# Performance work log

Hardware: AMD Instinct MI355X
Metric: run time of the kernel (lower is better)

Reference implementation:

```python
import jax, jax.numpy as jnp
import numpy as np

N, F_IN, H, W = 8192, 512, 256, 64
THRESHOLD = 0.8


def setup_inputs() -> dict:
    key = jax.random.key(0)
    ks = jax.random.split(key, 9)
    def lin(k, fan_in, shape):
        return (jax.random.normal(k, shape, jnp.float32) / np.sqrt(fan_in)).astype(jnp.float32)
    return {
        "state_batch": jax.random.normal(ks[0], (N, F_IN), jnp.float32),
        "W1": lin(ks[1], F_IN, (F_IN, H)), "b1": jnp.zeros((H,), jnp.float32),
        "W2": lin(ks[2], H, (H, H)),      "b2": jnp.zeros((H,), jnp.float32),
        "Wq": lin(ks[3], H, (H, W)),      "bq": jnp.zeros((W,), jnp.float32),
        "Wh": lin(ks[4], W, (W, 1)),      "bh": jnp.zeros((1,), jnp.float32),
    }


def reference(state_batch, W1, b1, W2, b2, Wq, bq, Wh, bh):
    # classical encoder: two ReLU Linear layers
    enc = jax.nn.relu(state_batch @ W1 + b1)
    enc = jax.nn.relu(enc @ W2 + b2)
    # quantum layer surrogate: bounded features in [-1, 1] like PauliZ expectations
    q_out = jnp.tanh(enc @ Wq + bq)                      # [N, W]

    # pairwise squared-cosine fidelity (vectorized Gram matrix, replaces
    # the itertools.combinations + .item() host-sync loop)
    qn = q_out / (jnp.linalg.norm(q_out, axis=1, keepdims=True) + 1e-12)
    fid = (qn @ qn.T) ** 2                               # [N, N]

    n = q_out.shape[0]
    # graph edges: fid >= threshold, no self loops; edge weight = 1.0
    mask = (fid >= THRESHOLD) & (~jnp.eye(n, dtype=bool))
    deg = mask.sum(axis=1)
    wsum = mask.astype(q_out.dtype).sum(axis=1)          # all weights are 1.0
    # mean neighbor weight; nodes with no neighbors keep their own feature (factor 1)
    mean_w = jnp.where(deg > 0, wsum / jnp.maximum(deg, 1).astype(q_out.dtype), 1.0)
    attn = q_out * mean_w[:, None]                       # [N, W]

    agg = attn.sum(axis=0, keepdims=True)                # [1, W]
    out = (agg @ Wh + bh).squeeze(-1)                    # [1]
    return out
```

## Files before the change

kernel.cpp:

```cpp
#include <hip/hip_runtime.h>
#include <hip/hip_bf16.h>
#include <math.h>


#define N_ROWS 8192
#define F_IN   512
#define H_DIM  256
#define W_DIM  64

#define LDW 72
#define LDE 280

#define W1_E (F_IN * H_DIM)
#define W2_E (H_DIM * H_DIM)
#define WQ_E (H_DIM * W_DIM)
#define W_BLOCKS ((W1_E + W2_E + WQ_E + 255) / 256)

using bf16x8 = __attribute__((ext_vector_type(8))) short;
using bf16x4 = __attribute__((ext_vector_type(4))) short;
using f32x4  = __attribute__((ext_vector_type(4))) float;
typedef __hip_bfloat16 bf16;

__device__ __forceinline__ void split2(float v, bf16& hi, bf16& lo) {
    bf16 h = __float2bfloat16(v);
    hi = h;
    lo = __float2bfloat16(v - __bfloat162float(h));
}

__global__ __launch_bounds__(256) void prep_w(
    const float* __restrict__ W1, const float* __restrict__ W2,
    const float* __restrict__ Wq, const float* __restrict__ bh,
    bf16* __restrict__ W1h, bf16* __restrict__ W1l,
    bf16* __restrict__ W2h, bf16* __restrict__ W2l,
    bf16* __restrict__ Wqh, bf16* __restrict__ Wql,
    float* __restrict__ out)
{
    if (blockIdx.x == 0 && threadIdx.x == 0) out[0] = bh[0];
    int gid = blockIdx.x * 256 + threadIdx.x;
    if (gid < W1_E) {
        int k = gid >> 8, n = gid & 255;
        split2(W1[gid], W1h[n * F_IN + k], W1l[n * F_IN + k]);
        return;
    }
    gid -= W1_E;
    if (gid < W2_E) {
        int k = gid >> 8, n = gid & 255;
        split2(W2[gid], W2h[n * H_DIM + k], W2l[n * H_DIM + k]);
        return;
    }
    gid -= W2_E;
    if (gid < WQ_E) {
        int k = gid >> 6, n = gid & 63;
        split2(Wq[gid], Wqh[n * H_DIM + k], Wql[n * H_DIM + k]);
    }
}

__global__ __launch_bounds__(512) void fused_chain(
    const float* __restrict__ S,
    const bf16* __restrict__ W1h, const bf16* __restrict__ W1l,
    const bf16* __restrict__ W2h, const bf16* __restrict__ W2l,
    const bf16* __restrict__ Wqh, const bf16* __restrict__ Wql,
    const float* __restrict__ b1, const float* __restrict__ b2,
    const float* __restrict__ bq, const float* __restrict__ Wh,
    float* __restrict__ out)
{
    __shared__ bf16 Ssh[32 * LDW];
    __shared__ bf16 Ssl[32 * LDW];
    __shared__ bf16 Bsh[256 * LDW];
    __shared__ bf16 Bsl[256 * LDW];
    __shared__ bf16 E1h[32 * LDE];
    __shared__ bf16 E1l[32 * LDE];
    __shared__ bf16 E2h[32 * LDE];
    __shared__ bf16 E2l[32 * LDE];
    __shared__ float red[2][64];

    const int t = threadIdx.x;
    const int w = t >> 6, quad = (t & 63) >> 4, m16 = t & 15;
    const int row0 = blockIdx.x * 32;

    f32x4 acc[2][2] = {};
    {
        const int srow = t >> 4, scol = (t & 15) << 2;
        float4 sv;
        bf16x8 wv[8];
        sv = *(const float4*)(S + (size_t)(row0 + srow) * F_IN + scol);
        #pragma unroll
        for (int i = 0; i < 8; ++i) {
            const int c = t + 512 * i, pl = c >> 11, cp = c & 2047;
            const int n = cp >> 3, sg = (cp & 7) << 3;
            wv[i] = *(const bf16x8*)((pl ? W1l : W1h) + (size_t)n * F_IN + sg);
        }
        for (int k0 = 0; k0 < F_IN; k0 += 64) {
            __syncthreads();
            {
                bf16 hb[4], lb[4];
                split2(sv.x, hb[0], lb[0]); split2(sv.y, hb[1], lb[1]);
                split2(sv.z, hb[2], lb[2]); split2(sv.w, hb[3], lb[3]);
                *(bf16x4*)&Ssh[srow * LDW + scol] = *(const bf16x4*)hb;
                *(bf16x4*)&Ssl[srow * LDW + scol] = *(const bf16x4*)lb;
            }
            #pragma unroll
            for (int i = 0; i < 8; ++i) {
                const int c = t + 512 * i, pl = c >> 11, cp = c & 2047;
                const int n = cp >> 3, sg = (cp & 7) << 3;
                *(bf16x8*)&(pl ? Bsl : Bsh)[n * LDW + sg] = wv[i];
            }
            __syncthreads();
            if (k0 + 64 < F_IN) {
                sv = *(const float4*)(S + (size_t)(row0 + srow) * F_IN + k0 + 64 + scol);
                #pragma unroll
                for (int i = 0; i < 8; ++i) {
                    const int c = t + 512 * i, pl = c >> 11, cp = c & 2047;
                    const int n = cp >> 3, sg = (cp & 7) << 3;
                    wv[i] = *(const bf16x8*)((pl ? W1l : W1h) + (size_t)n * F_IN + k0 + 64 + sg);
                }
            }
            #pragma unroll
            for (int kk = 0; kk < 64; kk += 32) {
                bf16x8 a0h = *(const bf16x8*)(&Ssh[m16 * LDW + kk + quad * 8]);
                bf16x8 a0l = *(const bf16x8*)(&Ssl[m16 * LDW + kk + quad * 8]);
                bf16x8 a1h = *(const bf16x8*)(&Ssh[(16 + m16) * LDW + kk + quad * 8]);
                bf16x8 a1l = *(const bf16x8*)(&Ssl[(16 + m16) * LDW + kk + quad * 8]);
                #pragma unroll
                for (int jj = 0; jj < 2; ++jj) {
                    const int bn = (32 * w + jj * 16 + m16) * LDW + kk + quad * 8;
                    bf16x8 b_h = *(const bf16x8*)(&Bsh[bn]);
                    bf16x8 b_l = *(const bf16x8*)(&Bsl[bn]);
                    acc[0][jj] = __builtin_amdgcn_mfma_f32_16x16x32_bf16(a0h, b_h, acc[0][jj], 0, 0, 0);
                    acc[0][jj] = __builtin_amdgcn_mfma_f32_16x16x32_bf16(a0l, b_h, acc[0][jj], 0, 0, 0);
                    acc[0][jj] = __builtin_amdgcn_mfma_f32_16x16x32_bf16(a0h, b_l, acc[0][jj], 0, 0, 0);
                    acc[1][jj] = __builtin_amdgcn_mfma_f32_16x16x32_bf16(a1h, b_h, acc[1][jj], 0, 0, 0);
                    acc[1][jj] = __builtin_amdgcn_mfma_f32_16x16x32_bf16(a1l, b_h, acc[1][jj], 0, 0, 0);
                    acc[1][jj] = __builtin_amdgcn_mfma_f32_16x16x32_bf16(a1h, b_l, acc[1][jj], 0, 0, 0);
                }
            }
        }
        #pragma unroll
        for (int i = 0; i < 2; ++i)
            #pragma unroll
            for (int jj = 0; jj < 2; ++jj) {
                const int c = 32 * w + jj * 16 + m16;
                const float bv = b1[c];
                #pragma unroll
                for (int r = 0; r < 4; ++r) {
                    const int rr = i * 16 + quad * 4 + r;
                    float vv = fmaxf(acc[i][jj][r] + bv, 0.0f);
                    split2(vv, E1h[rr * LDE + c], E1l[rr * LDE + c]);
                }
            }
    }

    {
        bf16x8 wv[8];
        #pragma unroll
        for (int i = 0; i < 8; ++i) {
            const int c = t + 512 * i, pl = c >> 11, cp = c & 2047;
            const int n = cp >> 3, sg = (cp & 7) << 3;
            wv[i] = *(const bf16x8*)((pl ? W2l : W2h) + (size_t)n * H_DIM + sg);
        }
        #pragma unroll
        for (int i = 0; i < 2; ++i)
            #pragma unroll
            for (int jj = 0; jj < 2; ++jj)
                acc[i][jj] = (f32x4){0.f, 0.f, 0.f, 0.f};
        for (int k0 = 0; k0 < H_DIM; k0 += 64) {
            __syncthreads();
            #pragma unroll
            for (int i = 0; i < 8; ++i) {
                const int c = t + 512 * i, pl = c >> 11, cp = c & 2047;
                const int n = cp >> 3, sg = (cp & 7) << 3;
                *(bf16x8*)&(pl ? Bsl : Bsh)[n * LDW + sg] = wv[i];
            }
            __syncthreads();
            if (k0 + 64 < H_DIM) {
                #pragma unroll
                for (int i = 0; i < 8; ++i) {
                    const int c = t + 512 * i, pl = c >> 11, cp = c & 2047;
                    const int n = cp >> 3, sg = (cp & 7) << 3;
                    wv[i] = *(const bf16x8*)((pl ? W2l : W2h) + (size_t)n * H_DIM + k0 + 64 + sg);
                }
            }
            #pragma unroll
            for (int kk = 0; kk < 64; kk += 32) {
                bf16x8 a0h = *(const bf16x8*)(&E1h[m16 * LDE + k0 + kk + quad * 8]);
                bf16x8 a0l = *(const bf16x8*)(&E1l[m16 * LDE + k0 + kk + quad * 8]);
                bf16x8 a1h = *(const bf16x8*)(&E1h[(16 + m16) * LDE + k0 + kk + quad * 8]);
                bf16x8 a1l = *(const bf16x8*)(&E1l[(16 + m16) * LDE + k0 + kk + quad * 8]);
                #pragma unroll
                for (int jj = 0; jj < 2; ++jj) {
                    const int bn = (32 * w + jj * 16 + m16) * LDW + kk + quad * 8;
                    bf16x8 b_h = *(const bf16x8*)(&Bsh[bn]);
                    bf16x8 b_l = *(const bf16x8*)(&Bsl[bn]);
                    acc[0][jj] = __builtin_amdgcn_mfma_f32_16x16x32_bf16(a0h, b_h, acc[0][jj], 0, 0, 0);
                    acc[0][jj] = __builtin_amdgcn_mfma_f32_16x16x32_bf16(a0l, b_h, acc[0][jj], 0, 0, 0);
                    acc[0][jj] = __builtin_amdgcn_mfma_f32_16x16x32_bf16(a0h, b_l, acc[0][jj], 0, 0, 0);
                    acc[1][jj] = __builtin_amdgcn_mfma_f32_16x16x32_bf16(a1h, b_h, acc[1][jj], 0, 0, 0);
                    acc[1][jj] = __builtin_amdgcn_mfma_f32_16x16x32_bf16(a1l, b_h, acc[1][jj], 0, 0, 0);
                    acc[1][jj] = __builtin_amdgcn_mfma_f32_16x16x32_bf16(a1h, b_l, acc[1][jj], 0, 0, 0);
                }
            }
        }
        #pragma unroll
        for (int i = 0; i < 2; ++i)
            #pragma unroll
            for (int jj = 0; jj < 2; ++jj) {
                const int c = 32 * w + jj * 16 + m16;
                const float bv = b2[c];
                #pragma unroll
                for (int r = 0; r < 4; ++r) {
                    const int rr = i * 16 + quad * 4 + r;
                    float vv = fmaxf(acc[i][jj][r] + bv, 0.0f);
                    split2(vv, E2h[rr * LDE + c], E2l[rr * LDE + c]);
                }
            }
    }

    {
        const int rf = w >> 2, cf = w & 3;
        f32x4 acc3 = {0.f, 0.f, 0.f, 0.f};
        bf16x8 wq[2];
        #pragma unroll
        for (int i = 0; i < 2; ++i) {
            const int c = t + 512 * i, pl = c >> 9, cp = c & 511;
            const int n = cp >> 3, sg = (cp & 7) << 3;
            wq[i] = *(const bf16x8*)((pl ? Wql : Wqh) + (size_t)n * H_DIM + sg);
        }
        for (int k0 = 0; k0 < H_DIM; k0 += 64) {
            __syncthreads();
            #pragma unroll
            for (int i = 0; i < 2; ++i) {
                const int c = t + 512 * i, pl = c >> 9, cp = c & 511;
                const int n = cp >> 3, sg = (cp & 7) << 3;
                *(bf16x8*)&(pl ? Bsl : Bsh)[n * LDW + sg] = wq[i];
            }
            __syncthreads();
            if (k0 + 64 < H_DIM) {
                #pragma unroll
                for (int i = 0; i < 2; ++i) {
                    const int c = t + 512 * i, pl = c >> 9, cp = c & 511;
                    const int n = cp >> 3, sg = (cp & 7) << 3;
                    wq[i] = *(const bf16x8*)((pl ? Wql : Wqh) + (size_t)n * H_DIM + k0 + 64 + sg);
                }
            }
            #pragma unroll
            for (int kk = 0; kk < 64; kk += 32) {
                bf16x8 a_h = *(const bf16x8*)(&E2h[(rf * 16 + m16) * LDE + k0 + kk + quad * 8]);
                bf16x8 a_l = *(const bf16x8*)(&E2l[(rf * 16 + m16) * LDE + k0 + kk + quad * 8]);
                const int bn = (cf * 16 + m16) * LDW + kk + quad * 8;
                bf16x8 b_h = *(const bf16x8*)(&Bsh[bn]);
                bf16x8 b_l = *(const bf16x8*)(&Bsl[bn]);
                acc3 = __builtin_amdgcn_mfma_f32_16x16x32_bf16(a_h, b_h, acc3, 0, 0, 0);
                acc3 = __builtin_amdgcn_mfma_f32_16x16x32_bf16(a_l, b_h, acc3, 0, 0, 0);
                acc3 = __builtin_amdgcn_mfma_f32_16x16x32_bf16(a_h, b_l, acc3, 0, 0, 0);
            }
        }
        const int c = cf * 16 + m16;
        const float bv = bq[c];
        float v = 0.f;
        #pragma unroll
        for (int r = 0; r < 4; ++r)
            v += tanhf(acc3[r] + bv);
        v += __shfl_xor(v, 16, 64);
        v += __shfl_xor(v, 32, 64);
        if (quad == 0) red[rf][c] = v;
        __syncthreads();
        if (t < W_DIM) {
            float s = (red[0][t] + red[1][t]) * Wh[t];
            #pragma unroll
            for (int o = 32; o > 0; o >>= 1) s += __shfl_down(s, o);
            if (t == 0) atomicAdd(out, s);
        }
    }
}

extern "C" void kernel_launch(void* const* d_in, const int* in_sizes, int n_in,
                              void* d_out, int out_size, void* d_ws, size_t ws_size,
                              hipStream_t stream) {
    const float* state = (const float*)d_in[0];
    const float* W1    = (const float*)d_in[1];
    const float* b1    = (const float*)d_in[2];
    const float* W2    = (const float*)d_in[3];
    const float* b2    = (const float*)d_in[4];
    const float* Wq    = (const float*)d_in[5];
    const float* bq    = (const float*)d_in[6];
    const float* Wh    = (const float*)d_in[7];
    const float* bh    = (const float*)d_in[8];

    bf16* p = (bf16*)d_ws;
    bf16* W1h = p; p += (size_t)H_DIM * F_IN;
    bf16* W1l = p; p += (size_t)H_DIM * F_IN;
    bf16* W2h = p; p += (size_t)H_DIM * H_DIM;
    bf16* W2l = p; p += (size_t)H_DIM * H_DIM;
    bf16* Wqh = p; p += (size_t)W_DIM * H_DIM;
    bf16* Wql = p; p += (size_t)W_DIM * H_DIM;

    prep_w<<<W_BLOCKS, 256, 0, stream>>>(
        W1, W2, Wq, bh, W1h, W1l, W2h, W2l, Wqh, Wql, (float*)d_out);

    fused_chain<<<N_ROWS / 32, 512, 0, stream>>>(
        state, W1h, W1l, W2h, W2l, Wqh, Wql, b1, b2, bq, Wh, (float*)d_out);
}
```

Before: 101.4 us.

## Pre-swizzle weights into MFMA fragment order and read B directly from global

The weight prep kernel now writes the bf16 hi/lo weight splits in per-lane MFMA fragment order, so each lane can load its B operand as one contiguous 16-byte global read. The fused chain no longer stages weights through shared memory. It loads the full 32x512 state tile into LDS once and then runs the K loops with no per-step barriers. This removes LDS staging traffic and most __syncthreads, in exchange for more global/L2 weight reads per block and less explicit prefetch overlap. The layout change also frees LDS, which could allow higher occupancy.

```diff
diff --git a/kernel.cpp b/kernel.cpp
--- a/kernel.cpp
+++ b/kernel.cpp
@@ -8,13 +8,14 @@
 #define H_DIM  256
 #define W_DIM  64
 
-#define LDW 72
-#define LDE 280
-
-#define W1_E (F_IN * H_DIM)
-#define W2_E (H_DIM * H_DIM)
-#define WQ_E (H_DIM * W_DIM)
-#define W_BLOCKS ((W1_E + W2_E + WQ_E + 255) / 256)
+#define LDS_S 520
+#define LDE   264
+
+#define W1_FRAGS (16 * 16 * 64)
+#define W2_FRAGS (16 * 8 * 64)
+#define WQ_FRAGS (4 * 8 * 64)
+#define PREP_T   (W1_FRAGS + W2_FRAGS + WQ_FRAGS)
+#define PREP_BLOCKS ((PREP_T + 255) / 256)
 
 using bf16x8 = __attribute__((ext_vector_type(8))) short;
 using bf16x4 = __attribute__((ext_vector_type(4))) short;
@@ -37,21 +38,42 @@
 {
     if (blockIdx.x == 0 && threadIdx.x == 0) out[0] = bh[0];
     int gid = blockIdx.x * 256 + threadIdx.x;
-    if (gid < W1_E) {
-        int k = gid >> 8, n = gid & 255;
-        split2(W1[gid], W1h[n * F_IN + k], W1l[n * F_IN + k]);
+    if (gid < W1_FRAGS) {
+        const int l = gid & 63, ks = (gid >> 6) & 15, n16 = gid >> 10;
+        const int n = n16 * 16 + (l & 15);
+        const int kb = ks * 32 + ((l >> 4) << 3);
+        bf16 hb[8], lb[8];
+        #pragma unroll
+        for (int j = 0; j < 8; ++j)
+            split2(W1[(size_t)(kb + j) * H_DIM + n], hb[j], lb[j]);
+        *(bf16x8*)(W1h + (size_t)gid * 8) = *(const bf16x8*)hb;
+        *(bf16x8*)(W1l + (size_t)gid * 8) = *(const bf16x8*)lb;
         return;
     }
-    gid -= W1_E;
-    if (gid < W2_E) {
-        int k = gid >> 8, n = gid & 255;
-        split2(W2[gid], W2h[n * H_DIM + k], W2l[n * H_DIM + k]);
+    gid -= W1_FRAGS;
+    if (gid < W2_FRAGS) {
+        const int l = gid & 63, ks = (gid >> 6) & 7, n16 = gid >> 9;
+        const int n = n16 * 16 + (l & 15);
+        const int kb = ks * 32 + ((l >> 4) << 3);
+        bf16 hb[8], lb[8];
+        #pragma unroll
+        for (int j = 0; j < 8; ++j)
+            split2(W2[(size_t)(kb + j) * H_DIM + n], hb[j], lb[j]);
+        *(bf16x8*)(W2h + (size_t)gid * 8) = *(const bf16x8*)hb;
+        *(bf16x8*)(W2l + (size_t)gid * 8) = *(const bf16x8*)lb;
         return;
     }
-    gid -= W2_E;
-    if (gid < WQ_E) {
-        int k = gid >> 6, n = gid & 63;
-        split2(Wq[gid], Wqh[n * H_DIM + k], Wql[n * H_DIM + k]);
+    gid -= W2_FRAGS;
+    if (gid < WQ_FRAGS) {
+        const int l = gid & 63, ks = (gid >> 6) & 7, n16 = gid >> 9;
+        const int n = n16 * 16 + (l & 15);
+        const int kb = ks * 32 + ((l >> 4) << 3);
+        bf16 hb[8], lb[8];
+        #pragma unroll
+        for (int j = 0; j < 8; ++j)
+            split2(Wq[(size_t)(kb + j) * W_DIM + n], hb[j], lb[j]);
+        *(bf16x8*)(Wqh + (size_t)gid * 8) = *(const bf16x8*)hb;
+        *(bf16x8*)(Wql + (size_t)gid * 8) = *(const bf16x8*)lb;
     }
 }
 
@@ -64,10 +86,8 @@
     const float* __restrict__ bq, const float* __restrict__ Wh,
     float* __restrict__ out)
 {
-    __shared__ bf16 Ssh[32 * LDW];
-    __shared__ bf16 Ssl[32 * LDW];
-    __shared__ bf16 Bsh[256 * LDW];
-    __shared__ bf16 Bsl[256 * LDW];
+    __shared__ bf16 Ssh[32 * LDS_S];
+    __shared__ bf16 Ssl[32 * LDS_S];
     __shared__ bf16 E1h[32 * LDE];
     __shared__ bf16 E1l[32 * LDE];
     __shared__ bf16 E2h[32 * LDE];
@@ -75,184 +95,113 @@
     __shared__ float red[2][64];
 
     const int t = threadIdx.x;
-    const int w = t >> 6, quad = (t & 63) >> 4, m16 = t & 15;
+    const int lane = t & 63;
+    const int w = t >> 6, quad = lane >> 4, m16 = t & 15;
     const int row0 = blockIdx.x * 32;
 
+    #pragma unroll
+    for (int i = 0; i < 8; ++i) {
+        const int idx = i * 2048 + t * 4;
+        const int r = idx >> 9, c = idx & 511;
+        float4 sv = *(const float4*)(S + (size_t)(row0 + r) * F_IN + c);
+        bf16 hb[4], lb[4];
+        split2(sv.x, hb[0], lb[0]); split2(sv.y, hb[1], lb[1]);
+        split2(sv.z, hb[2], lb[2]); split2(sv.w, hb[3], lb[3]);
+        *(bf16x4*)&Ssh[r * LDS_S + c] = *(const bf16x4*)hb;
+        *(bf16x4*)&Ssl[r * LDS_S + c] = *(const bf16x4*)lb;
+    }
+    __syncthreads();
+
     f32x4 acc[2][2] = {};
-    {
-        const int srow = t >> 4, scol = (t & 15) << 2;
-        float4 sv;
-        bf16x8 wv[8];
-        sv = *(const float4*)(S + (size_t)(row0 + srow) * F_IN + scol);
-        #pragma unroll
-        for (int i = 0; i < 8; ++i) {
-            const int c = t + 512 * i, pl = c >> 11, cp = c & 2047;
-            const int n = cp >> 3, sg = (cp & 7) << 3;
-            wv[i] = *(const bf16x8*)((pl ? W1l : W1h) + (size_t)n * F_IN + sg);
-        }
-        for (int k0 = 0; k0 < F_IN; k0 += 64) {
-            __syncthreads();
-            {
-                bf16 hb[4], lb[4];
-                split2(sv.x, hb[0], lb[0]); split2(sv.y, hb[1], lb[1]);
-                split2(sv.z, hb[2], lb[2]); split2(sv.w, hb[3], lb[3]);
-                *(bf16x4*)&Ssh[srow * LDW + scol] = *(const bf16x4*)hb;
-                *(bf16x4*)&Ssl[srow * LDW + scol] = *(const bf16x4*)lb;
+    #pragma unroll
+    for (int ks = 0; ks < F_IN / 32; ++ks) {
+        const int ao = ks * 32 + quad * 8;
+        bf16x8 a0h = *(const bf16x8*)&Ssh[m16 * LDS_S + ao];
+        bf16x8 a0l = *(const bf16x8*)&Ssl[m16 * LDS_S + ao];
+        bf16x8 a1h = *(const bf16x8*)&Ssh[(16 + m16) * LDS_S + ao];
+        bf16x8 a1l = *(const bf16x8*)&Ssl[(16 + m16) * LDS_S + ao];
+        #pragma unroll
+        for (int jj = 0; jj < 2; ++jj) {
+            const size_t off = ((size_t)(((2 * w + jj) * 16 + ks) * 64 + lane)) * 8;
+            bf16x8 b_h = *(const bf16x8*)(W1h + off);
+            bf16x8 b_l = *(const bf16x8*)(W1l + off);
+            acc[0][jj] = __builtin_amdgcn_mfma_f32_16x16x32_bf16(a0h, b_h, acc[0][jj], 0, 0, 0);
+            acc[0][jj] = __builtin_amdgcn_mfma_f32_16x16x32_bf16(a0l, b_h, acc[0][jj], 0, 0, 0);
+            acc[0][jj] = __builtin_amdgcn_mfma_f32_16x16x32_bf16(a0h, b_l, acc[0][jj], 0, 0, 0);
+            acc[1][jj] = __builtin_amdgcn_mfma_f32_16x16x32_bf16(a1h, b_h, acc[1][jj], 0, 0, 0);
+            acc[1][jj] = __builtin_amdgcn_mfma_f32_16x16x32_bf16(a1l, b_h, acc[1][jj], 0, 0, 0);
+            acc[1][jj] = __builtin_amdgcn_mfma_f32_16x16x32_bf16(a1h, b_l, acc[1][jj], 0, 0, 0);
+        }
+    }
+    #pragma unroll
+    for (int i = 0; i < 2; ++i)
+        #pragma unroll
+        for (int jj = 0; jj < 2; ++jj) {
+            const int c = 32 * w + jj * 16 + m16;
+            const float bv = b1[c];
+            #pragma unroll
+            for (int r = 0; r < 4; ++r) {
+                const int rr = i * 16 + quad * 4 + r;
+                float vv = fmaxf(acc[i][jj][r] + bv, 0.0f);
+                split2(vv, E1h[rr * LDE + c], E1l[rr * LDE + c]);
             }
+        }
+    __syncthreads();
+
+    #pragma unroll
+    for (int i = 0; i < 2; ++i)
+        #pragma unroll
+        for (int jj = 0; jj < 2; ++jj)
+            acc[i][jj] = (f32x4){0.f, 0.f, 0.f, 0.f};
+    #pragma unroll
+    for (int ks = 0; ks < H_DIM / 32; ++ks) {
+        const int ao = ks * 32 + quad * 8;
+        bf16x8 a0h = *(const bf16x8*)&E1h[m16 * LDE + ao];
+        bf16x8 a0l = *(const bf16x8*)&E1l[m16 * LDE + ao];
+        bf16x8 a1h = *(const bf16x8*)&E1h[(16 + m16) * LDE + ao];
+        bf16x8 a1l = *(const bf16x8*)&E1l[(16 + m16) * LDE + ao];
+        #pragma unroll
+        for (int jj = 0; jj < 2; ++jj) {
+            const size_t off = ((size_t)(((2 * w + jj) * 8 + ks) * 64 + lane)) * 8;
+            bf16x8 b_h = *(const bf16x8*)(W2h + off);
+            bf16x8 b_l = *(const bf16x8*)(W2l + off);
+            acc[0][jj] = __builtin_amdgcn_mfma_f32_16x16x32_bf16(a0h, b_h, acc[0][jj], 0, 0, 0);
+            acc[0][jj] = __builtin_amdgcn_mfma_f32_16x16x32_bf16(a0l, b_h, acc[0][jj], 0, 0, 0);
+            acc[0][jj] = __builtin_amdgcn_mfma_f32_16x16x32_bf16(a0h, b_l, acc[0][jj], 0, 0, 0);
+            acc[1][jj] = __builtin_amdgcn_mfma_f32_16x16x32_bf16(a1h, b_h, acc[1][jj], 0, 0, 0);
+            acc[1][jj] = __builtin_amdgcn_mfma_f32_16x16x32_bf16(a1l, b_h, acc[1][jj], 0, 0, 0);
+            acc[1][jj] = __builtin_amdgcn_mfma_f32_16x16x32_bf16(a1h, b_l, acc[1][jj], 0, 0, 0);
+        }
+    }
+    #pragma unroll
+    for (int i = 0; i < 2; ++i)
+        #pragma unroll
+        for (int jj = 0; jj < 2; ++jj) {
+            const int c = 32 * w + jj * 16 + m16;
+            const float bv = b2[c];
             #pragma unroll
-            for (int i = 0; i < 8; ++i) {
-                const int c = t + 512 * i, pl = c >> 11, cp = c & 2047;
-                const int n = cp >> 3, sg = (cp & 7) << 3;
-                *(bf16x8*)&(pl ? Bsl : Bsh)[n * LDW + sg] = wv[i];
+            for (int r = 0; r < 4; ++r) {
+                const int rr = i * 16 + quad * 4 + r;
+                float vv = fmaxf(acc[i][jj][r] + bv, 0.0f);
+                split2(vv, E2h[rr * LDE + c], E2l[rr * LDE + c]);
             }
-            __syncthreads();
-            if (k0 + 64 < F_IN) {
-                sv = *(const float4*)(S + (size_t)(row0 + srow) * F_IN + k0 + 64 + scol);
-                #pragma unroll
-                for (int i = 0; i < 8; ++i) {
-                    const int c = t + 512 * i, pl = c >> 11, cp = c & 2047;
-                    const int n = cp >> 3, sg = (cp & 7) << 3;
-                    wv[i] = *(const bf16x8*)((pl ? W1l : W1h) + (size_t)n * F_IN + k0 + 64 + sg);
-                }
-            }
-            #pragma unroll
-            for (int kk = 0; kk < 64; kk += 32) {
-                bf16x8 a0h = *(const bf16x8*)(&Ssh[m16 * LDW + kk + quad * 8]);
-                bf16x8 a0l = *(const bf16x8*)(&Ssl[m16 * LDW + kk + quad * 8]);
-                bf16x8 a1h = *(const bf16x8*)(&Ssh[(16 + m16) * LDW + kk + quad * 8]);
-                bf16x8 a1l = *(const bf16x8*)(&Ssl[(16 + m16) * LDW + kk + quad * 8]);
-                #pragma unroll
-                for (int jj = 0; jj < 2; ++jj) {
-                    const int bn = (32 * w + jj * 16 + m16) * LDW + kk + quad * 8;
-                    bf16x8 b_h = *(const bf16x8*)(&Bsh[bn]);
-                    bf16x8 b_l = *(const bf16x8*)(&Bsl[bn]);
-                    acc[0][jj] = __builtin_amdgcn_mfma_f32_16x16x32_bf16(a0h, b_h, acc[0][jj], 0, 0, 0);
-                    acc[0][jj] = __builtin_amdgcn_mfma_f32_16x16x32_bf16(a0l, b_h, acc[0][jj], 0, 0, 0);
-                    acc[0][jj] = __builtin_amdgcn_mfma_f32_16x16x32_bf16(a0h, b_l, acc[0][jj], 0, 0, 0);
-                    acc[1][jj] = __builtin_amdgcn_mfma_f32_16x16x32_bf16(a1h, b_h, acc[1][jj], 0, 0, 0);
-                    acc[1][jj] = __builtin_amdgcn_mfma_f32_16x16x32_bf16(a1l, b_h, acc[1][jj], 0, 0, 0);
-                    acc[1][jj] = __builtin_amdgcn_mfma_f32_16x16x32_bf16(a1h, b_l, acc[1][jj], 0, 0, 0);
-                }
-            }
-        }
-        #pragma unroll
-        for (int i = 0; i < 2; ++i)
-            #pragma unroll
-            for (int jj = 0; jj < 2; ++jj) {
-                const int c = 32 * w + jj * 16 + m16;
-                const float bv = b1[c];
-                #pragma unroll
-                for (int r = 0; r < 4; ++r) {
-                    const int rr = i * 16 + quad * 4 + r;
-                    float vv = fmaxf(acc[i][jj][r] + bv, 0.0f);
-                    split2(vv, E1h[rr * LDE + c], E1l[rr * LDE + c]);
-                }
-            }
-    }
-
-    {
-        bf16x8 wv[8];
-        #pragma unroll
-        for (int i = 0; i < 8; ++i) {
-            const int c = t + 512 * i, pl = c >> 11, cp = c & 2047;
-            const int n = cp >> 3, sg = (cp & 7) << 3;
-            wv[i] = *(const bf16x8*)((pl ? W2l : W2h) + (size_t)n * H_DIM + sg);
-        }
-        #pragma unroll
-        for (int i = 0; i < 2; ++i)
-            #pragma unroll
-            for (int jj = 0; jj < 2; ++jj)
-                acc[i][jj] = (f32x4){0.f, 0.f, 0.f, 0.f};
-        for (int k0 = 0; k0 < H_DIM; k0 += 64) {
-            __syncthreads();
-            #pragma unroll
-            for (int i = 0; i < 8; ++i) {
-                const int c = t + 512 * i, pl = c >> 11, cp = c & 2047;
-                const int n = cp >> 3, sg = (cp & 7) << 3;
-                *(bf16x8*)&(pl ? Bsl : Bsh)[n * LDW + sg] = wv[i];
-            }
-            __syncthreads();
-            if (k0 + 64 < H_DIM) {
-                #pragma unroll
-                for (int i = 0; i < 8; ++i) {
-                    const int c = t + 512 * i, pl = c >> 11, cp = c & 2047;
-                    const int n = cp >> 3, sg = (cp & 7) << 3;
-                    wv[i] = *(const bf16x8*)((pl ? W2l : W2h) + (size_t)n * H_DIM + k0 + 64 + sg);
-                }
-            }
-            #pragma unroll
-            for (int kk = 0; kk < 64; kk += 32) {
-                bf16x8 a0h = *(const bf16x8*)(&E1h[m16 * LDE + k0 + kk + quad * 8]);
-                bf16x8 a0l = *(const bf16x8*)(&E1l[m16 * LDE + k0 + kk + quad * 8]);
-                bf16x8 a1h = *(const bf16x8*)(&E1h[(16 + m16) * LDE + k0 + kk + quad * 8]);
-                bf16x8 a1l = *(const bf16x8*)(&E1l[(16 + m16) * LDE + k0 + kk + quad * 8]);
-                #pragma unroll
-                for (int jj = 0; jj < 2; ++jj) {
-                    const int bn = (32 * w + jj * 16 + m16) * LDW + kk + quad * 8;
-                    bf16x8 b_h = *(const bf16x8*)(&Bsh[bn]);
-                    bf16x8 b_l = *(const bf16x8*)(&Bsl[bn]);
-                    acc[0][jj] = __builtin_amdgcn_mfma_f32_16x16x32_bf16(a0h, b_h, acc[0][jj], 0, 0, 0);
-                    acc[0][jj] = __builtin_amdgcn_mfma_f32_16x16x32_bf16(a0l, b_h, acc[0][jj], 0, 0, 0);
-                    acc[0][jj] = __builtin_amdgcn_mfma_f32_16x16x32_bf16(a0h, b_l, acc[0][jj], 0, 0, 0);
-                    acc[1][jj] = __builtin_amdgcn_mfma_f32_16x16x32_bf16(a1h, b_h, acc[1][jj], 0, 0, 0);
-                    acc[1][jj] = __builtin_amdgcn_mfma_f32_16x16x32_bf16(a1l, b_h, acc[1][jj], 0, 0, 0);
-                    acc[1][jj] = __builtin_amdgcn_mfma_f32_16x16x32_bf16(a1h, b_l, acc[1][jj], 0, 0, 0);
-                }
-            }
-        }
-        #pragma unroll
-        for (int i = 0; i < 2; ++i)
-            #pragma unroll
-            for (int jj = 0; jj < 2; ++jj) {
-                const int c = 32 * w + jj * 16 + m16;
-                const float bv = b2[c];
-                #pragma unroll
-                for (int r = 0; r < 4; ++r) {
-                    const int rr = i * 16 + quad * 4 + r;
-                    float vv = fmaxf(acc[i][jj][r] + bv, 0.0f);
-                    split2(vv, E2h[rr * LDE + c], E2l[rr * LDE + c]);
-                }
-            }
-    }
+        }
+    __syncthreads();
 
     {
         const int rf = w >> 2, cf = w & 3;
         f32x4 acc3 = {0.f, 0.f, 0.f, 0.f};
-        bf16x8 wq[2];
-        #pragma unroll
-        for (int i = 0; i < 2; ++i) {
-            const int c = t + 512 * i, pl = c >> 9, cp = c & 511;
-            const int n = cp >> 3, sg = (cp & 7) << 3;
-            wq[i] = *(const bf16x8*)((pl ? Wql : Wqh) + (size_t)n * H_DIM + sg);
-        }
-        for (int k0 = 0; k0 < H_DIM; k0 += 64) {
-            __syncthreads();
-            #pragma unroll
-            for (int i = 0; i < 2; ++i) {
-                const int c = t + 512 * i, pl = c >> 9, cp = c & 511;
-                const int n = cp >> 3, sg = (cp & 7) << 3;
-                *(bf16x8*)&(pl ? Bsl : Bsh)[n * LDW + sg] = wq[i];
-            }
-            __syncthreads();
-            if (k0 + 64 < H_DIM) {
-                #pragma unroll
-                for (int i = 0; i < 2; ++i) {
-                    const int c = t + 512 * i, pl = c >> 9, cp = c & 511;
-                    const int n = cp >> 3, sg = (cp & 7) << 3;
-                    wq[i] = *(const bf16x8*)((pl ? Wql : Wqh) + (size_t)n * H_DIM + k0 + 64 + sg);
-                }
-            }
-            #pragma unroll
-            for (int kk = 0; kk < 64; kk += 32) {
-                bf16x8 a_h = *(const bf16x8*)(&E2h[(rf * 16 + m16) * LDE + k0 + kk + quad * 8]);
-                bf16x8 a_l = *(const bf16x8*)(&E2l[(rf * 16 + m16) * LDE + k0 + kk + quad * 8]);
-                const int bn = (cf * 16 + m16) * LDW + kk + quad * 8;
-                bf16x8 b_h = *(const bf16x8*)(&Bsh[bn]);
-                bf16x8 b_l = *(const bf16x8*)(&Bsl[bn]);
-                acc3 = __builtin_amdgcn_mfma_f32_16x16x32_bf16(a_h, b_h, acc3, 0, 0, 0);
-                acc3 = __builtin_amdgcn_mfma_f32_16x16x32_bf16(a_l, b_h, acc3, 0, 0, 0);
-                acc3 = __builtin_amdgcn_mfma_f32_16x16x32_bf16(a_h, b_l, acc3, 0, 0, 0);
-            }
+        #pragma unroll
+        for (int ks = 0; ks < H_DIM / 32; ++ks) {
+            const int ao = ks * 32 + quad * 8;
+            bf16x8 a_h = *(const bf16x8*)&E2h[(rf * 16 + m16) * LDE + ao];
+            bf16x8 a_l = *(const bf16x8*)&E2l[(rf * 16 + m16) * LDE + ao];
+            const size_t off = ((size_t)((cf * 8 + ks) * 64 + lane)) * 8;
+            bf16x8 b_h = *(const bf16x8*)(Wqh + off);
+            bf16x8 b_l = *(const bf16x8*)(Wql + off);
+            acc3 = __builtin_amdgcn_mfma_f32_16x16x32_bf16(a_h, b_h, acc3, 0, 0, 0);
+            acc3 = __builtin_amdgcn_mfma_f32_16x16x32_bf16(a_l, b_h, acc3, 0, 0, 0);
+            acc3 = __builtin_amdgcn_mfma_f32_16x16x32_bf16(a_h, b_l, acc3, 0, 0, 0);
         }
         const int c = cf * 16 + m16;
         const float bv = bq[c];
@@ -294,7 +243,7 @@
     bf16* Wqh = p; p += (size_t)W_DIM * H_DIM;
     bf16* Wql = p; p += (size_t)W_DIM * H_DIM;
 
-    prep_w<<<W_BLOCKS, 256, 0, stream>>>(
+    prep_w<<<PREP_BLOCKS, 256, 0, stream>>>(
         W1, W2, Wq, bh, W1h, W1l, W2h, W2l, Wqh, Wql, (float*)d_out);
 
     fused_chain<<<N_ROWS / 32, 512, 0, stream>>>(
```

Result: faster. 97.37 us (-4.0%).
